# Performance work log

Measured on AMD Instinct MI355X. Metric: run time of the kernel, lower is better.

## Reference

```python
import jax, jax.numpy as jnp
import numpy as np

P = 100_000      # distinct products
T = 300_000      # total product nodes after repeat_interleave (sum of cnt)
NQ = 100_000     # query nodes
B = 8192         # number of sessions (segments)
QIN = 128; PIN = 128; D = 128; MSL = 50; DL = D - MSL


def setup_inputs() -> dict:
    key = jax.random.key(0)
    ks = jax.random.split(key, 12)
    # irregular repeat counts in {1..5}, tiled so sum == 3*P == T exactly (static shape)
    cnt = jnp.asarray(np.tile(np.array([1, 2, 3, 4, 5], np.int32), P // 5))
    s = 0.05
    return {
        "query_feat": jax.random.normal(ks[0], (NQ, QIN), jnp.float32),
        "product_feat": jax.random.normal(ks[1], (P, PIN), jnp.float32),
        "Wq": jax.random.normal(ks[2], (DL, QIN), jnp.float32) * s,
        "bq": jnp.zeros((DL,), jnp.float32),
        "Wp": jax.random.normal(ks[3], (DL, PIN), jnp.float32) * s,
        "bp": jnp.zeros((DL,), jnp.float32),
        "pos_table": jax.random.normal(ks[4], (MSL, MSL), jnp.float32) * s,
        "Wn": jax.random.normal(ks[5], (D, D), jnp.float32) * s,
        "bn": jnp.zeros((D,), jnp.float32),
        "Wc": jax.random.normal(ks[6], (D, D), jnp.float32) * s,
        "Wa": jax.random.normal(ks[7], (1, D), jnp.float32) * s,
        "query_pos_id": jax.random.randint(ks[8], (NQ,), 0, MSL, jnp.int32),
        "product_pos_id": jax.random.randint(ks[9], (T,), 0, MSL, jnp.int32),
        "query_batch": jax.random.randint(ks[10], (NQ,), 0, B, jnp.int32),
        "product_batch": jax.random.randint(ks[11], (P,), 0, B, jnp.int32),
        "cnt": cnt,
        "num_segments": B,
        "total_product_nodes": T,
    }


def _segment_mean(x, seg, num_segments):
    sums = jax.ops.segment_sum(x, seg, num_segments=num_segments)
    counts = jax.ops.segment_sum(jnp.ones((x.shape[0],), x.dtype), seg, num_segments=num_segments)
    return sums / jnp.maximum(counts, 1.0)[:, None]


def reference(query_feat, product_feat, Wq, bq, Wp, bp, pos_table, Wn, bn, Wc, Wa,
              query_pos_id, product_pos_id, query_batch, product_batch, cnt,
              num_segments, total_product_nodes):
    # query branch: linear -> concat positional embedding -> tanh  [NQ, D]
    qe = jnp.tanh(jnp.concatenate([query_feat @ Wq.T + bq, pos_table[query_pos_id]], axis=1))
    # product branch: linear, repeat_interleave by cnt, concat pos emb, tanh  [T, D]
    pe = product_feat @ Wp.T + bp
    pe = jnp.repeat(pe, cnt, axis=0, total_repeat_length=total_product_nodes)
    pe = jnp.tanh(jnp.concatenate([pe, pos_table[product_pos_id]], axis=1))
    pbatch = jnp.repeat(product_batch, cnt, axis=0, total_repeat_length=total_product_nodes)
    # stack nodes (products first, then queries — matches torch.concat order)
    node_emb = jnp.concatenate([pe, qe], axis=0)            # [N, D]
    node_batch = jnp.concatenate([pbatch, query_batch], axis=0)
    # coarse session representation: segment mean, broadcast back to nodes
    coarse = _segment_mean(node_emb, node_batch, num_segments)  # [B, D]
    coarse_g = coarse[node_batch]                                # [N, D]
    # attention gating
    att = jax.nn.sigmoid(node_emb @ Wn.T + bn + coarse_g @ Wc.T) @ Wa.T  # [N, 1]
    weighted = node_emb * att
    return _segment_mean(weighted, node_batch, num_segments)    # [B, D]
```

## Files before the change

kernel.cpp:

```cpp
#include <hip/hip_runtime.h>
#include <hip/hip_bf16.h>
#include <math.h>


constexpr int D   = 128;
constexpr int DL  = 78;
constexpr int MSL = 50;
constexpr int RP  = 80;

typedef __attribute__((ext_vector_type(8))) short bfrag8;
typedef __attribute__((ext_vector_type(4))) float facc4;
typedef __attribute__((ext_vector_type(4))) short short4v;

__device__ __forceinline__ float sigmoidf_(float x) {
    return 1.f / (1.f + __expf(-x));
}
__device__ __forceinline__ float ftanh(float x) {
    float e = __expf(2.f * x);
    return 1.f - 2.f * __builtin_amdgcn_rcpf(e + 1.f);
}

__device__ __forceinline__ char* ldsAddr(__hip_bfloat16* base, int row, int byte_in_row) {
    return reinterpret_cast<char*>(base) + row * 256 + (byte_in_row ^ ((row & 7) << 4));
}
__device__ __forceinline__ bfrag8 ldsR16(const __hip_bfloat16* base, int row, int byte_in_row) {
    return *reinterpret_cast<const bfrag8*>(
        reinterpret_cast<const char*>(base) + row * 256 + (byte_in_row ^ ((row & 7) << 4)));
}
__device__ __forceinline__ short4v ldsR8(const __hip_bfloat16* base, int row, int byte_in_row) {
    return *reinterpret_cast<const short4v*>(
        reinterpret_cast<const char*>(base) + row * 256 + (byte_in_row ^ ((row & 7) << 4)));
}

__device__ __forceinline__ bfrag8 cvt8(float4 a, float4 b) {
    __hip_bfloat16 t[8] = {__float2bfloat16(a.x), __float2bfloat16(a.y),
                           __float2bfloat16(a.z), __float2bfloat16(a.w),
                           __float2bfloat16(b.x), __float2bfloat16(b.y),
                           __float2bfloat16(b.z), __float2bfloat16(b.w)};
    return *reinterpret_cast<bfrag8*>(t);
}

__global__ __launch_bounds__(256) void k_tables2(
    const float* __restrict__ pos_table, const float* __restrict__ Wn,
    float* __restrict__ tpos, float* __restrict__ posWn) {
    __shared__ float tposL[MSL * MSL];
    int t = threadIdx.x;
    for (int o = t; o < MSL * MSL; o += 256) tposL[o] = tanhf(pos_table[o]);
    __syncthreads();
    if (blockIdx.x == 0)
        for (int o = t; o < MSL * MSL; o += 256) tpos[o] = tposL[o];
    for (int o = blockIdx.x * 256 + t; o < MSL * D; o += gridDim.x * 256) {
        int r = o >> 7, d = o & 127;
        float acc = 0.f;
        #pragma unroll 10
        for (int j = 0; j < MSL; ++j) acc += tposL[r * MSL + j] * Wn[d * D + DL + j];
        posWn[o] = acc;
    }
}

__global__ __launch_bounds__(256) void k_convW(
    const float* __restrict__ Wq, const float* __restrict__ Wp, const float* __restrict__ Wn,
    __hip_bfloat16* __restrict__ Wqbf, __hip_bfloat16* __restrict__ Wpbf,
    __hip_bfloat16* __restrict__ Wnbf) {
    int i = blockIdx.x * 256 + threadIdx.x;
    if (i < 80 * 128) {
        int n = i >> 7;
        Wqbf[i] = __float2bfloat16((n < DL) ? Wq[i] : 0.f);
        Wpbf[i] = __float2bfloat16((n < DL) ? Wp[i] : 0.f);
    } else if (i < 80 * 128 + 128 * 128) {
        int o = i - 80 * 128;
        int j = o & 127;
        Wnbf[o] = __float2bfloat16((j < DL) ? Wn[o] : 0.f);
    }
}

__global__ void k_scanA(const int* __restrict__ cnt, int P, int* __restrict__ chunkSum) {
    __shared__ int s[256];
    int p = blockIdx.x * 256 + threadIdx.x;
    s[threadIdx.x] = (p < P) ? cnt[p] : 0;
    __syncthreads();
    for (int st = 128; st > 0; st >>= 1) {
        if (threadIdx.x < st) s[threadIdx.x] += s[threadIdx.x + st];
        __syncthreads();
    }
    if (threadIdx.x == 0) chunkSum[blockIdx.x] = s[0];
}
__global__ __launch_bounds__(1024) void k_scanB(
    const int* __restrict__ chunkSum, int nC, int* __restrict__ chunkOff) {
    __shared__ int s[1024];
    int t = threadIdx.x;
    int carry = 0;
    for (int base = 0; base < nC; base += 1024) {
        int v = (base + t < nC) ? chunkSum[base + t] : 0;
        s[t] = v;
        __syncthreads();
        for (int st = 1; st < 1024; st <<= 1) {
            int add = (t >= st) ? s[t - st] : 0;
            __syncthreads();
            s[t] += add;
            __syncthreads();
        }
        if (base + t < nC) chunkOff[base + t] = carry + s[t] - v;
        carry += s[1023];
        __syncthreads();
    }
}
__global__ void k_scanC(const int* __restrict__ cnt, int P, const int* __restrict__ chunkOff,
                        int* __restrict__ prodOff) {
    __shared__ int s[256];
    int t = threadIdx.x;
    int p = blockIdx.x * 256 + t;
    int v = (p < P) ? cnt[p] : 0;
    s[t] = v;
    __syncthreads();
    for (int st = 1; st < 256; st <<= 1) {
        int add = (t >= st) ? s[t - st] : 0;
        __syncthreads();
        s[t] += add;
        __syncthreads();
    }
    if (p < P) prodOff[p] = chunkOff[blockIdx.x] + s[t] - v;
}

__global__ void k_cnt2(const int* __restrict__ qbatch, const int* __restrict__ pbatch,
                       const int* __restrict__ cnt, int NQ, int P, int* __restrict__ nodeCnt) {
    int i = blockIdx.x * 256 + threadIdx.x;
    if (i < NQ) {
        atomicAdd(&nodeCnt[qbatch[i]], 1);
    } else if (i < NQ + P) {
        int p = i - NQ;
        atomicAdd(&nodeCnt[pbatch[p]], cnt[p]);
    }
}
__global__ __launch_bounds__(1024) void k_scanSeg(
    const int* __restrict__ nodeCnt, int B, int* __restrict__ segOff, int* __restrict__ cursor) {
    __shared__ int s[1024];
    int t = threadIdx.x;
    int carry = 0;
    for (int base = 0; base < B; base += 1024) {
        int v = (base + t < B) ? nodeCnt[base + t] : 0;
        s[t] = v;
        __syncthreads();
        for (int st = 1; st < 1024; st <<= 1) {
            int add = (t >= st) ? s[t - st] : 0;
            __syncthreads();
            s[t] += add;
            __syncthreads();
        }
        if (base + t < B) {
            int e = carry + s[t] - v;
            segOff[base + t] = e;
            cursor[base + t] = e;
        }
        carry += s[1023];
        __syncthreads();
    }
    if (t == 0) segOff[B] = carry;
}
__global__ void k_rank2(const int* __restrict__ qbatch, const int* __restrict__ pbatch,
                        const int* __restrict__ qpos, const int* __restrict__ ppos,
                        const int* __restrict__ cnt, const int* __restrict__ prodOff,
                        int NQ, int P, int* __restrict__ cursor, int* __restrict__ nodeIdx) {
    int i = blockIdx.x * 256 + threadIdx.x;
    if (i < NQ) {
        int slot = atomicAdd(&cursor[qbatch[i]], 1);
        nodeIdx[slot] = (i << 6) | qpos[i];
    } else if (i < NQ + P) {
        int p = i - NQ;
        int c = cnt[p], off = prodOff[p];
        int slot = atomicAdd(&cursor[pbatch[p]], c);
        for (int j = 0; j < c; ++j)
            nodeIdx[slot + j] = ((NQ + p) << 6) | ppos[off + j];
    }
}

__global__ __launch_bounds__(256) void k_branch2(
    const float* __restrict__ qfeat, const float* __restrict__ pfeat,
    const __hip_bfloat16* __restrict__ Wqbf, const __hip_bfloat16* __restrict__ Wpbf,
    const float* __restrict__ bq, const float* __restrict__ bp,
    const __hip_bfloat16* __restrict__ Wnbf,
    int NQ, int P, int qBlocks,
    __hip_bfloat16* __restrict__ tEU, __hip_bfloat16* __restrict__ eWnU) {
    const bool isQ = (int)blockIdx.x < qBlocks;
    const int r0 = (isQ ? blockIdx.x : blockIdx.x - qBlocks) * 64;
    const float* feat = isQ ? qfeat : pfeat;
    const __hip_bfloat16* Wbf = isQ ? Wqbf : Wpbf;
    const float* bias = isQ ? bq : bp;
    const int Nrows = isQ ? NQ : P;
    const int rowBase = isQ ? 0 : NQ;

    __shared__ __hip_bfloat16 linL[64 * 128];
    __shared__ __hip_bfloat16 eWnL[64 * 128];
    int t = threadIdx.x;
    int l = t & 63, w = t >> 6;
    int lr = l & 15, lq = l >> 4;
    int am = w * 16 + lr;

    if (l < 16) {
        bfrag8 z = {0, 0, 0, 0, 0, 0, 0, 0};
        *reinterpret_cast<bfrag8*>(ldsAddr(linL, w * 16 + l, 160)) = z;
        *reinterpret_cast<bfrag8*>(ldsAddr(linL, w * 16 + l, 176)) = z;
    }

    int gra = r0 + am;
    const float* frow = &feat[(size_t)(gra < Nrows ? gra : Nrows - 1) * 128];
    bfrag8 a[4];
    #pragma unroll
    for (int kt = 0; kt < 4; ++kt) {
        float4 u = *reinterpret_cast<const float4*>(&frow[kt * 32 + lq * 8]);
        float4 v = *reinterpret_cast<const float4*>(&frow[kt * 32 + lq * 8 + 4]);
        a[kt] = cvt8(u, v);
    }

    facc4 c1[5];
    #pragma unroll
    for (int nt = 0; nt < 5; ++nt) { facc4 z = {0.f, 0.f, 0.f, 0.f}; c1[nt] = z; }
    #pragma unroll
    for (int nt = 0; nt < 5; ++nt) {
        #pragma unroll
        for (int kt = 0; kt < 4; ++kt) {
            bfrag8 b = *reinterpret_cast<const bfrag8*>(&Wbf[(nt * 16 + lr) * 128 + kt * 32 + lq * 8]);
            c1[nt] = __builtin_amdgcn_mfma_f32_16x16x32_bf16(a[kt], b, c1[nt], 0, 0, 0);
        }
    }

    #pragma unroll
    for (int nt = 0; nt < 5; ++nt) {
        int n = nt * 16 + lr;
        float bs = (n < DL) ? bias[n] : 0.f;
        #pragma unroll
        for (int j = 0; j < 4; ++j) {
            int m = w * 16 + lq * 4 + j;
            float tv = (n < DL) ? ftanh(c1[nt][j] + bs) : 0.f;
            *reinterpret_cast<__hip_bfloat16*>(ldsAddr(linL, m, 2 * n)) = __float2bfloat16(tv);
        }
    }

    {
        int r = w * 16 + (l >> 2), c = l & 3;
        int gr = r0 + r;
        #pragma unroll
        for (int j = 0; j < 5; ++j) {
            short4v v = ldsR8(linL, r, c * 40 + j * 8);
            if (gr < Nrows)
                *reinterpret_cast<short4v*>(&tEU[(size_t)(rowBase + gr) * RP + c * 20 + j * 4]) = v;
        }
    }

    bfrag8 a2[3];
    #pragma unroll
    for (int kt = 0; kt < 3; ++kt) a2[kt] = ldsR16(linL, am, kt * 64 + lq * 16);
    facc4 c2[8];
    #pragma unroll
    for (int nt = 0; nt < 8; ++nt) { facc4 z = {0.f, 0.f, 0.f, 0.f}; c2[nt] = z; }
    #pragma unroll
    for (int nt = 0; nt < 8; ++nt) {
        #pragma unroll
        for (int kt = 0; kt < 3; ++kt) {
            bfrag8 b = *reinterpret_cast<const bfrag8*>(&Wnbf[(nt * 16 + lr) * 128 + kt * 32 + lq * 8]);
            c2[nt] = __builtin_amdgcn_mfma_f32_16x16x32_bf16(a2[kt], b, c2[nt], 0, 0, 0);
        }
    }
    #pragma unroll
    for (int nt = 0; nt < 8; ++nt) {
        int d2 = nt * 16 + lr;
        #pragma unroll
        for (int j = 0; j < 4; ++j) {
            int m = w * 16 + lq * 4 + j;
            *reinterpret_cast<__hip_bfloat16*>(ldsAddr(eWnL, m, 2 * d2)) =
                __float2bfloat16(c2[nt][j]);
        }
    }
    {
        int r = w * 16 + (l >> 2), c = l & 3;
        int gr = r0 + r;
        #pragma unroll
        for (int j = 0; j < 4; ++j) {
            bfrag8 v = ldsR16(eWnL, r, c * 64 + j * 16);
            if (gr < Nrows)
                *reinterpret_cast<bfrag8*>(&eWnU[(size_t)(rowBase + gr) * 128 + c * 32 + j * 8]) = v;
        }
    }
}

__global__ __launch_bounds__(128) void k_segsum3(
    const __hip_bfloat16* __restrict__ tEU, const int* __restrict__ nodeIdx,
    const int* __restrict__ segOff, const float* __restrict__ tpos, int B,
    float* __restrict__ segsum, float* __restrict__ segcnt) {
    int b = blockIdx.x, t = threadIdx.x;
    int s0 = segOff[b], s1 = segOff[b + 1];
    float acc = 0.f;
    if (t < DL) {
        for (int i = s0; i < s1; i += 4) {
            #pragma unroll
            for (int j = 0; j < 4; ++j) {
                if (i + j < s1) {
                    int row = nodeIdx[i + j] >> 6;
                    acc += __bfloat162float(tEU[(size_t)row * RP + t]);
                }
            }
        }
        segsum[(size_t)b * D + t] = acc;
    } else {
        int k = t - DL;
        for (int i = s0; i < s1; i += 4) {
            #pragma unroll
            for (int j = 0; j < 4; ++j) {
                if (i + j < s1) {
                    int pos = nodeIdx[i + j] & 63;
                    acc += tpos[pos * MSL + k];
                }
            }
        }
        segsum[(size_t)b * D + DL + k] = acc;
        if (k == 0) segcnt[b] = (float)(s1 - s0);
    }
}

__global__ __launch_bounds__(256) void k_coarse(
    const float* __restrict__ segsum, const float* __restrict__ segcnt,
    const float* __restrict__ Wc, const float* __restrict__ bn, int B,
    float* __restrict__ coarseWc) {
    __shared__ __hip_bfloat16 WcL[128 * 130];
    __shared__ float cL[16 * 128];
    int t = threadIdx.x;
    int b0 = blockIdx.x * 16;
    for (int o = t; o < D * D; o += 256) {
        int d = o >> 7, k = o & 127;
        WcL[d * 130 + k] = __float2bfloat16(Wc[o]);
    }
    for (int o = t; o < 16 * D; o += 256) {
        int bb = o >> 7, d = o & 127;
        int b = b0 + bb;
        cL[o] = (b < B) ? segsum[(size_t)b * D + d] / fmaxf(segcnt[b], 1.f) : 0.f;
    }
    __syncthreads();
    for (int o = t; o < 16 * D; o += 256) {
        int bb = o >> 7, d = o & 127;
        int b = b0 + bb;
        if (b >= B) continue;
        float acc = bn[d];
        const float* cr = &cL[bb * 128];
        const __hip_bfloat16* wr = &WcL[d * 130];
        #pragma unroll 8
        for (int j = 0; j < D; ++j) acc += cr[j] * __bfloat162float(wr[j]);
        coarseWc[(size_t)b * D + d] = acc;
    }
}

__global__ __launch_bounds__(256) void k_att4(
    const __hip_bfloat16* __restrict__ eWnU, const __hip_bfloat16* __restrict__ tEU,
    const float* __restrict__ coarseWc, const float* __restrict__ posWn,
    const float* __restrict__ tpos, const float* __restrict__ Wa,
    const int* __restrict__ nodeIdx, const int* __restrict__ segOff,
    const float* __restrict__ segcnt, int B, float* __restrict__ out) {
    int wv = threadIdx.x >> 6, l = threadIdx.x & 63;
    int b = blockIdx.x * 4 + wv;
    if (b >= B) return;

    float cw0 = coarseWc[(size_t)b * D + l];
    float cw1 = coarseWc[(size_t)b * D + 64 + l];
    float wa0 = Wa[l], wa1 = Wa[64 + l];
    float acc0 = 0.f, acc1 = 0.f, posacc = 0.f;
    int s0 = segOff[b], s1 = segOff[b + 1];

    for (int i = s0; i < s1; i += 8) {
        float part[8];
        int   row[8], pos[8];
        #pragma unroll
        for (int j = 0; j < 8; ++j) {
            bool on = (i + j) < s1;
            int pk = on ? nodeIdx[i + j] : 0;
            row[j] = pk >> 6;
            pos[j] = pk & 63;
            float z0 = __bfloat162float(eWnU[(size_t)row[j] * D + l])      + cw0 + posWn[pos[j] * D + l];
            float z1 = __bfloat162float(eWnU[(size_t)row[j] * D + 64 + l]) + cw1 + posWn[pos[j] * D + 64 + l];
            part[j] = on ? (sigmoidf_(z0) * wa0 + sigmoidf_(z1) * wa1) : 0.f;
        }
        #pragma unroll
        for (int m = 1; m < 64; m <<= 1) {
            #pragma unroll
            for (int j = 0; j < 8; ++j) part[j] += __shfl_xor(part[j], m, 64);
        }
        #pragma unroll
        for (int j = 0; j < 8; ++j) {
            acc0 += part[j] * __bfloat162float(tEU[(size_t)row[j] * RP + l]);
            if (l < 14) acc1 += part[j] * __bfloat162float(tEU[(size_t)row[j] * RP + 64 + l]);
            else        posacc += part[j] * tpos[pos[j] * MSL + (l - 14)];
        }
    }

    float inv = 1.f / fmaxf(segcnt[b], 1.f);
    out[(size_t)b * D + l] = acc0 * inv;
    out[(size_t)b * D + 64 + l] = (l < 14 ? acc1 : posacc) * inv;
}

extern "C" void kernel_launch(void* const* d_in, const int* in_sizes, int n_in,
                              void* d_out, int out_size, void* d_ws, size_t ws_size,
                              hipStream_t stream) {
    const float* query_feat   = (const float*)d_in[0];
    const float* product_feat = (const float*)d_in[1];
    const float* Wq = (const float*)d_in[2];
    const float* bq = (const float*)d_in[3];
    const float* Wp = (const float*)d_in[4];
    const float* bp = (const float*)d_in[5];
    const float* pos_table = (const float*)d_in[6];
    const float* Wn = (const float*)d_in[7];
    const float* bn = (const float*)d_in[8];
    const float* Wc = (const float*)d_in[9];
    const float* Wa = (const float*)d_in[10];
    const int* qpos   = (const int*)d_in[11];
    const int* ppos   = (const int*)d_in[12];
    const int* qbatch = (const int*)d_in[13];
    const int* pbatch = (const int*)d_in[14];
    const int* cnt    = (const int*)d_in[15];

    int NQ = in_sizes[11];
    int T  = in_sizes[12];
    int P  = in_sizes[15];
    int B  = out_size / D;
    int NR = NQ + P;
    int NN = NQ + T;
    float* out = (float*)d_out;

    char* w = (char*)d_ws;
    size_t off = 0;
    auto take = [&](size_t bytes) -> char* {
        char* p = w + off;
        off = (off + bytes + 255) & ~(size_t)255;
        return p;
    };
    int*   nodeCnt = (int*)  take((size_t)B * 4);
    size_t zeroBytes = off;
    float* segsum   = (float*)take((size_t)B * D * 4);
    float* segcnt   = (float*)take((size_t)B * 4);
    float* coarseWc = (float*)take((size_t)B * D * 4);
    float* tpos  = (float*)take(MSL * MSL * 4);
    float* posWn = (float*)take(MSL * D * 4);
    __hip_bfloat16* Wqbf = (__hip_bfloat16*)take(80 * 128 * 2);
    __hip_bfloat16* Wpbf = (__hip_bfloat16*)take(80 * 128 * 2);
    __hip_bfloat16* Wnbf = (__hip_bfloat16*)take(128 * 128 * 2);
    int nC = (P + 255) / 256;
    int* chunkSum = (int*)take((size_t)nC * 4);
    int* chunkOff = (int*)take((size_t)nC * 4);
    int* prodOff  = (int*)take((size_t)P * 4);
    int* segOffA  = (int*)take((size_t)(B + 1) * 4);
    int* cursor   = (int*)take((size_t)B * 4);
    int* nodeIdx  = (int*)take((size_t)NN * 4);
    __hip_bfloat16* tEU  = (__hip_bfloat16*)take((size_t)NR * RP * 2);
    __hip_bfloat16* eWnU = (__hip_bfloat16*)take((size_t)NR * D * 2);
    (void)ws_size; (void)n_in;

    hipMemsetAsync(nodeCnt, 0, zeroBytes, stream);

    hipLaunchKernelGGL(k_tables2, dim3(8), dim3(256), 0, stream, pos_table, Wn, tpos, posWn);
    hipLaunchKernelGGL(k_convW, dim3((80 * 128 + 128 * 128 + 255) / 256), dim3(256), 0, stream,
                       Wq, Wp, Wn, Wqbf, Wpbf, Wnbf);
    hipLaunchKernelGGL(k_scanA, dim3(nC), dim3(256), 0, stream, cnt, P, chunkSum);
    hipLaunchKernelGGL(k_scanB, dim3(1), dim3(1024), 0, stream, chunkSum, nC, chunkOff);
    hipLaunchKernelGGL(k_scanC, dim3(nC), dim3(256), 0, stream, cnt, P, chunkOff, prodOff);

    hipLaunchKernelGGL(k_cnt2, dim3((NR + 255) / 256), dim3(256), 0, stream,
                       qbatch, pbatch, cnt, NQ, P, nodeCnt);
    hipLaunchKernelGGL(k_scanSeg, dim3(1), dim3(1024), 0, stream, nodeCnt, B, segOffA, cursor);
    hipLaunchKernelGGL(k_rank2, dim3((NR + 255) / 256), dim3(256), 0, stream,
                       qbatch, pbatch, qpos, ppos, cnt, prodOff, NQ, P, cursor, nodeIdx);

    int qBlocks = (NQ + 63) / 64, pBlocksBr = (P + 63) / 64;
    hipLaunchKernelGGL(k_branch2, dim3(qBlocks + pBlocksBr), dim3(256), 0, stream,
                       query_feat, product_feat, Wqbf, Wpbf, bq, bp, Wnbf,
                       NQ, P, qBlocks, tEU, eWnU);

    hipLaunchKernelGGL(k_segsum3, dim3(B), dim3(128), 0, stream,
                       tEU, nodeIdx, segOffA, tpos, B, segsum, segcnt);
    hipLaunchKernelGGL(k_coarse, dim3((B + 15) / 16), dim3(256), 0, stream,
                       segsum, segcnt, Wc, bn, B, coarseWc);

    hipLaunchKernelGGL(k_att4, dim3((B + 3) / 4), dim3(256), 0, stream,
                       eWnU, tEU, coarseWc, posWn, tpos, Wa,
                       nodeIdx, segOffA, segcnt, B, out);
}
```

Baseline: 377.9 us.

## Split attention into node-parallel MFMA scoring kernel and per-segment pooling

The fused per-segment attention kernel is split in two. A node-parallel kernel computes each node's gate logits from bf16 eWn, coarse·Wc and pos·Wn tables, applies the sigmoid, and reduces against Wa with an MFMA, writing one attention scalar per node. A second per-segment kernel pools the embeddings weighted by these stored scalars. This removes the per-node cross-lane shuffle reductions and the load imbalance of walking long segments one wave at a time. In exchange it adds an extra launch, nodeSeg and att arrays, and lower precision from storing the sigmoid outputs and weight tables in bf16.

Result: faster. 322.8 us (-14.6%).

```diff
diff --git a/kernel.cpp b/kernel.cpp
--- a/kernel.cpp
+++ b/kernel.cpp
@@ -18,6 +18,13 @@
 __device__ __forceinline__ float ftanh(float x) {
     float e = __expf(2.f * x);
     return 1.f - 2.f * __builtin_amdgcn_rcpf(e + 1.f);
+}
+__device__ __forceinline__ float bs2f(short s) {
+    unsigned u = ((unsigned)(unsigned short)s) << 16;
+    return __builtin_bit_cast(float, u);
+}
+__device__ __forceinline__ short f2bs(float f) {
+    return __builtin_bit_cast(short, __float2bfloat16(f));
 }
 
 __device__ __forceinline__ char* ldsAddr(__hip_bfloat16* base, int row, int byte_in_row) {
@@ -42,7 +49,7 @@
 
 __global__ __launch_bounds__(256) void k_tables2(
     const float* __restrict__ pos_table, const float* __restrict__ Wn,
-    float* __restrict__ tpos, float* __restrict__ posWn) {
+    float* __restrict__ tpos, __hip_bfloat16* __restrict__ posWnbf) {
     __shared__ float tposL[MSL * MSL];
     int t = threadIdx.x;
     for (int o = t; o < MSL * MSL; o += 256) tposL[o] = tanhf(pos_table[o]);
@@ -54,14 +61,15 @@
         float acc = 0.f;
         #pragma unroll 10
         for (int j = 0; j < MSL; ++j) acc += tposL[r * MSL + j] * Wn[d * D + DL + j];
-        posWn[o] = acc;
+        posWnbf[o] = __float2bfloat16(acc);
     }
 }
 
 __global__ __launch_bounds__(256) void k_convW(
     const float* __restrict__ Wq, const float* __restrict__ Wp, const float* __restrict__ Wn,
+    const float* __restrict__ Wa,
     __hip_bfloat16* __restrict__ Wqbf, __hip_bfloat16* __restrict__ Wpbf,
-    __hip_bfloat16* __restrict__ Wnbf) {
+    __hip_bfloat16* __restrict__ Wnbf, __hip_bfloat16* __restrict__ Wabf) {
     int i = blockIdx.x * 256 + threadIdx.x;
     if (i < 80 * 128) {
         int n = i >> 7;
@@ -71,6 +79,9 @@
         int o = i - 80 * 128;
         int j = o & 127;
         Wnbf[o] = __float2bfloat16((j < DL) ? Wn[o] : 0.f);
+    } else if (i < 80 * 128 + 128 * 128 + 128) {
+        int o = i - 80 * 128 - 128 * 128;
+        Wabf[o] = __float2bfloat16(Wa[o]);
     }
 }
 
@@ -160,17 +171,23 @@
 __global__ void k_rank2(const int* __restrict__ qbatch, const int* __restrict__ pbatch,
                         const int* __restrict__ qpos, const int* __restrict__ ppos,
                         const int* __restrict__ cnt, const int* __restrict__ prodOff,
-                        int NQ, int P, int* __restrict__ cursor, int* __restrict__ nodeIdx) {
+                        int NQ, int P, int* __restrict__ cursor,
+                        int* __restrict__ nodeIdx, int* __restrict__ nodeSeg) {
     int i = blockIdx.x * 256 + threadIdx.x;
     if (i < NQ) {
-        int slot = atomicAdd(&cursor[qbatch[i]], 1);
+        int b = qbatch[i];
+        int slot = atomicAdd(&cursor[b], 1);
         nodeIdx[slot] = (i << 6) | qpos[i];
+        nodeSeg[slot] = b;
     } else if (i < NQ + P) {
         int p = i - NQ;
+        int b = pbatch[p];
         int c = cnt[p], off = prodOff[p];
-        int slot = atomicAdd(&cursor[pbatch[p]], c);
-        for (int j = 0; j < c; ++j)
+        int slot = atomicAdd(&cursor[b], c);
+        for (int j = 0; j < c; ++j) {
             nodeIdx[slot + j] = ((NQ + p) << 6) | ppos[off + j];
+            nodeSeg[slot + j] = b;
+        }
     }
 }
 
@@ -320,7 +337,7 @@
 __global__ __launch_bounds__(256) void k_coarse(
     const float* __restrict__ segsum, const float* __restrict__ segcnt,
     const float* __restrict__ Wc, const float* __restrict__ bn, int B,
-    float* __restrict__ coarseWc) {
+    __hip_bfloat16* __restrict__ cWcbf) {
     __shared__ __hip_bfloat16 WcL[128 * 130];
     __shared__ float cL[16 * 128];
     int t = threadIdx.x;
@@ -344,55 +361,83 @@
         const __hip_bfloat16* wr = &WcL[d * 130];
         #pragma unroll 8
         for (int j = 0; j < D; ++j) acc += cr[j] * __bfloat162float(wr[j]);
-        coarseWc[(size_t)b * D + d] = acc;
-    }
-}
-
-__global__ __launch_bounds__(256) void k_att4(
-    const __hip_bfloat16* __restrict__ eWnU, const __hip_bfloat16* __restrict__ tEU,
-    const float* __restrict__ coarseWc, const float* __restrict__ posWn,
-    const float* __restrict__ tpos, const float* __restrict__ Wa,
-    const int* __restrict__ nodeIdx, const int* __restrict__ segOff,
-    const float* __restrict__ segcnt, int B, float* __restrict__ out) {
+        cWcbf[(size_t)b * D + d] = __float2bfloat16(acc);
+    }
+}
+
+__global__ __launch_bounds__(256) void k_attw(
+    const __hip_bfloat16* __restrict__ eWnU, const __hip_bfloat16* __restrict__ cWcbf,
+    const __hip_bfloat16* __restrict__ posWnbf, const __hip_bfloat16* __restrict__ Wabf,
+    const int* __restrict__ nodeIdx, const int* __restrict__ nodeSeg,
+    int NN, float* __restrict__ att) {
+    int t = threadIdx.x;
+    int l = t & 63, w = t >> 6;
+    int lr = l & 15, lq = l >> 4;
+    int i0 = blockIdx.x * 64 + w * 16;
+    int n = i0 + lr;
+    bool on = n < NN;
+    int pk = on ? nodeIdx[n] : 0;
+    int b  = on ? nodeSeg[n] : 0;
+    int row = pk >> 6, pos = pk & 63;
+
+    facc4 c = {0.f, 0.f, 0.f, 0.f};
+    #pragma unroll
+    for (int kt = 0; kt < 4; ++kt) {
+        int col = kt * 32 + lq * 8;
+        bfrag8 e  = *reinterpret_cast<const bfrag8*>(&eWnU[(size_t)row * D + col]);
+        bfrag8 cw = *reinterpret_cast<const bfrag8*>(&cWcbf[(size_t)b * D + col]);
+        bfrag8 pw = *reinterpret_cast<const bfrag8*>(&posWnbf[pos * D + col]);
+        bfrag8 s;
+        #pragma unroll
+        for (int j = 0; j < 8; ++j) {
+            float z = bs2f(e[j]) + bs2f(cw[j]) + bs2f(pw[j]);
+            s[j] = f2bs(sigmoidf_(z));
+        }
+        bfrag8 wa = *reinterpret_cast<const bfrag8*>(&Wabf[col]);
+        c = __builtin_amdgcn_mfma_f32_16x16x32_bf16(s, wa, c, 0, 0, 0);
+    }
+    if (lr == 0) {
+        #pragma unroll
+        for (int j = 0; j < 4; ++j) {
+            int m = i0 + lq * 4 + j;
+            if (m < NN) att[m] = c[j];
+        }
+    }
+}
+
+__global__ __launch_bounds__(256) void k_pool(
+    const __hip_bfloat16* __restrict__ tEU, const float* __restrict__ att,
+    const float* __restrict__ tpos, const int* __restrict__ nodeIdx,
+    const int* __restrict__ segOff, const float* __restrict__ segcnt,
+    int B, float* __restrict__ out) {
     int wv = threadIdx.x >> 6, l = threadIdx.x & 63;
     int b = blockIdx.x * 4 + wv;
     if (b >= B) return;
-
-    float cw0 = coarseWc[(size_t)b * D + l];
-    float cw1 = coarseWc[(size_t)b * D + 64 + l];
-    float wa0 = Wa[l], wa1 = Wa[64 + l];
-    float acc0 = 0.f, acc1 = 0.f, posacc = 0.f;
     int s0 = segOff[b], s1 = segOff[b + 1];
-
-    for (int i = s0; i < s1; i += 8) {
-        float part[8];
-        int   row[8], pos[8];
-        #pragma unroll
-        for (int j = 0; j < 8; ++j) {
+    float acc0 = 0.f, acc1 = 0.f;
+
+    for (int i = s0; i < s1; i += 4) {
+        float a[4];
+        int row[4], pos[4];
+        #pragma unroll
+        for (int j = 0; j < 4; ++j) {
             bool on = (i + j) < s1;
             int pk = on ? nodeIdx[i + j] : 0;
+            a[j] = on ? att[i + j] : 0.f;
             row[j] = pk >> 6;
             pos[j] = pk & 63;
-            float z0 = __bfloat162float(eWnU[(size_t)row[j] * D + l])      + cw0 + posWn[pos[j] * D + l];
-            float z1 = __bfloat162float(eWnU[(size_t)row[j] * D + 64 + l]) + cw1 + posWn[pos[j] * D + 64 + l];
-            part[j] = on ? (sigmoidf_(z0) * wa0 + sigmoidf_(z1) * wa1) : 0.f;
-        }
-        #pragma unroll
-        for (int m = 1; m < 64; m <<= 1) {
-            #pragma unroll
-            for (int j = 0; j < 8; ++j) part[j] += __shfl_xor(part[j], m, 64);
-        }
-        #pragma unroll
-        for (int j = 0; j < 8; ++j) {
-            acc0 += part[j] * __bfloat162float(tEU[(size_t)row[j] * RP + l]);
-            if (l < 14) acc1 += part[j] * __bfloat162float(tEU[(size_t)row[j] * RP + 64 + l]);
-            else        posacc += part[j] * tpos[pos[j] * MSL + (l - 14)];
+        }
+        #pragma unroll
+        for (int j = 0; j < 4; ++j) {
+            acc0 += a[j] * __bfloat162float(tEU[(size_t)row[j] * RP + l]);
+            if (l < 14) acc1 += a[j] * __bfloat162float(tEU[(size_t)row[j] * RP + 64 + l]);
+            else        acc1 += a[j] * tpos[pos[j] * MSL + (l - 14)];
         }
     }
 
     float inv = 1.f / fmaxf(segcnt[b], 1.f);
     out[(size_t)b * D + l] = acc0 * inv;
-    out[(size_t)b * D + 64 + l] = (l < 14 ? acc1 : posacc) * inv;
+    out[(size_t)b * D + 64 + l] = acc1 * inv;
 }
 
 extern "C" void kernel_launch(void* const* d_in, const int* in_sizes, int n_in,
@@ -434,12 +479,13 @@
     size_t zeroBytes = off;
     float* segsum   = (float*)take((size_t)B * D * 4);
     float* segcnt   = (float*)take((size_t)B * 4);
-    float* coarseWc = (float*)take((size_t)B * D * 4);
     float* tpos  = (float*)take(MSL * MSL * 4);
-    float* posWn = (float*)take(MSL * D * 4);
+    __hip_bfloat16* posWnbf = (__hip_bfloat16*)take(MSL * D * 2);
+    __hip_bfloat16* cWcbf   = (__hip_bfloat16*)take((size_t)B * D * 2);
     __hip_bfloat16* Wqbf = (__hip_bfloat16*)take(80 * 128 * 2);
     __hip_bfloat16* Wpbf = (__hip_bfloat16*)take(80 * 128 * 2);
     __hip_bfloat16* Wnbf = (__hip_bfloat16*)take(128 * 128 * 2);
+    __hip_bfloat16* Wabf = (__hip_bfloat16*)take(128 * 2);
     int nC = (P + 255) / 256;
     int* chunkSum = (int*)take((size_t)nC * 4);
     int* chunkOff = (int*)take((size_t)nC * 4);
@@ -447,15 +493,17 @@
     int* segOffA  = (int*)take((size_t)(B + 1) * 4);
     int* cursor   = (int*)take((size_t)B * 4);
     int* nodeIdx  = (int*)take((size_t)NN * 4);
+    int* nodeSeg  = (int*)take((size_t)NN * 4);
+    float* att    = (float*)take((size_t)NN * 4);
     __hip_bfloat16* tEU  = (__hip_bfloat16*)take((size_t)NR * RP * 2);
     __hip_bfloat16* eWnU = (__hip_bfloat16*)take((size_t)NR * D * 2);
     (void)ws_size; (void)n_in;
 
     hipMemsetAsync(nodeCnt, 0, zeroBytes, stream);
 
-    hipLaunchKernelGGL(k_tables2, dim3(8), dim3(256), 0, stream, pos_table, Wn, tpos, posWn);
-    hipLaunchKernelGGL(k_convW, dim3((80 * 128 + 128 * 128 + 255) / 256), dim3(256), 0, stream,
-                       Wq, Wp, Wn, Wqbf, Wpbf, Wnbf);
+    hipLaunchKernelGGL(k_tables2, dim3(8), dim3(256), 0, stream, pos_table, Wn, tpos, posWnbf);
+    hipLaunchKernelGGL(k_convW, dim3((80 * 128 + 128 * 128 + 128 + 255) / 256), dim3(256), 0,
+                       stream, Wq, Wp, Wn, Wa, Wqbf, Wpbf, Wnbf, Wabf);
     hipLaunchKernelGGL(k_scanA, dim3(nC), dim3(256), 0, stream, cnt, P, chunkSum);
     hipLaunchKernelGGL(k_scanB, dim3(1), dim3(1024), 0, stream, chunkSum, nC, chunkOff);
     hipLaunchKernelGGL(k_scanC, dim3(nC), dim3(256), 0, stream, cnt, P, chunkOff, prodOff);
@@ -464,7 +512,8 @@
                        qbatch, pbatch, cnt, NQ, P, nodeCnt);
     hipLaunchKernelGGL(k_scanSeg, dim3(1), dim3(1024), 0, stream, nodeCnt, B, segOffA, cursor);
     hipLaunchKernelGGL(k_rank2, dim3((NR + 255) / 256), dim3(256), 0, stream,
-                       qbatch, pbatch, qpos, ppos, cnt, prodOff, NQ, P, cursor, nodeIdx);
+                       qbatch, pbatch, qpos, ppos, cnt, prodOff, NQ, P, cursor,
+                       nodeIdx, nodeSeg);
 
     int qBlocks = (NQ + 63) / 64, pBlocksBr = (P + 63) / 64;
     hipLaunchKernelGGL(k_branch2, dim3(qBlocks + pBlocksBr), dim3(256), 0, stream,
@@ -474,9 +523,10 @@
     hipLaunchKernelGGL(k_segsum3, dim3(B), dim3(128), 0, stream,
                        tEU, nodeIdx, segOffA, tpos, B, segsum, segcnt);
     hipLaunchKernelGGL(k_coarse, dim3((B + 15) / 16), dim3(256), 0, stream,
-                       segsum, segcnt, Wc, bn, B, coarseWc);
-
-    hipLaunchKernelGGL(k_att4, dim3((B + 3) / 4), dim3(256), 0, stream,
-                       eWnU, tEU, coarseWc, posWn, tpos, Wa,
-                       nodeIdx, segOffA, segcnt, B, out);
-}
+                       segsum, segcnt, Wc, bn, B, cWcbf);
+
+    hipLaunchKernelGGL(k_attw, dim3((NN + 63) / 64), dim3(256), 0, stream,
+                       eWnU, cWcbf, posWnbf, Wabf, nodeIdx, nodeSeg, NN, att);
+    hipLaunchKernelGGL(k_pool, dim3((B + 3) / 4), dim3(256), 0, stream,
+                       tEU, att, tpos, nodeIdx, segOffA, segcnt, B, out);
+}
```
